# Performance work log

Measured on AMD Instinct MI355X. Metric: run time of the kernel, lower is better.

## Reference

```python
import jax, jax.numpy as jnp
import numpy as np

B, C, H, W = 4, 256, 64, 64

def setup_inputs() -> dict:
    key = jax.random.key(0)
    ks = jax.random.split(key, 6)
    inv = 1.0 / np.sqrt(C)
    return {
        "feature": jax.random.normal(ks[0], (B, C, H, W), dtype=jnp.float32),
        "flow": jax.random.normal(ks[1], (B, 2, H, W), dtype=jnp.float32),
        "q_w": jax.random.uniform(ks[2], (C, C), dtype=jnp.float32, minval=-inv, maxval=inv),
        "q_b": jax.random.uniform(ks[3], (C,), dtype=jnp.float32, minval=-inv, maxval=inv),
        "k_w": jax.random.uniform(ks[4], (C, C), dtype=jnp.float32, minval=-inv, maxval=inv),
        "k_b": jax.random.uniform(ks[5], (C,), dtype=jnp.float32, minval=-inv, maxval=inv),
    }

def reference(feature, flow, q_w, q_b, k_w, k_b):
    b, c, h, w = feature.shape
    # [b,c,h,w] -> [b, h*w, c] tokens
    tok = feature.reshape(b, c, h * w).transpose(0, 2, 1)
    v = flow.reshape(b, 2, h * w).transpose(0, 2, 1)       # [b, hw, 2]
    q = jnp.einsum('bnc,dc->bnd', tok, q_w) + q_b           # Linear(c,c)
    k = jnp.einsum('bnc,dc->bnd', tok, k_w) + k_b
    scale = 1.0 / jnp.sqrt(jnp.asarray(c, dtype=q.dtype))
    scores = jnp.einsum('bld,bsd->bls', q, k) * scale       # [b, hw, hw]
    attn = jax.nn.softmax(scores, axis=-1)                  # dropout_p=0 -> no-op
    out = jnp.einsum('bls,bsv->blv', attn, v)               # [b, hw, 2]
    return out.reshape(b, h, w, 2).transpose(0, 3, 1, 2)    # [b, 2, h, w]
```

## Files before the change

### kernel.cpp

```cpp
#include <hip/hip_runtime.h>
#include <math.h>

#define BB 4
#define CC 256
#define HWN 4096
#define NTOK 16384
#define SCQ 0.09016844136f

typedef __attribute__((ext_vector_type(8))) short short8;
typedef __attribute__((ext_vector_type(4))) float f32x4;
typedef __attribute__((ext_vector_type(2))) float f32x2;
typedef unsigned short ushort_t;

__device__ __forceinline__ ushort_t f2bf(float f) {
    unsigned int u = __float_as_uint(f);
    unsigned int r = (u + 0x7FFFu + ((u >> 16) & 1u)) >> 16;
    return (ushort_t)r;
}
__device__ __forceinline__ unsigned int pack2(float a, float b) {
    return (unsigned int)f2bf(a) | ((unsigned int)f2bf(b) << 16);
}
__device__ __forceinline__ float fexp2(float x) {
#if __has_builtin(__builtin_amdgcn_exp2f)
    return __builtin_amdgcn_exp2f(x);
#else
    return exp2f(x);
#endif
}

__global__ __launch_bounds__(256) void prep_kernel(
    const float* __restrict__ feature,
    const float* __restrict__ q_w, const float* __restrict__ k_w,
    ushort_t* __restrict__ fbuf,
    ushort_t* __restrict__ qwb, ushort_t* __restrict__ kwb,
    float* __restrict__ zbuf)
{
    int bid = blockIdx.x;
    int tid = threadIdx.x;

    if (bid >= 1024) {
        int t = (bid - 1024) * 256 + tid;
        float4 q4 = *(const float4*)&q_w[(size_t)t * 4];
        float4 k4 = *(const float4*)&k_w[(size_t)t * 4];
        unsigned long long qo = (unsigned long long)pack2(q4.x * SCQ, q4.y * SCQ)
                              | ((unsigned long long)pack2(q4.z * SCQ, q4.w * SCQ) << 32);
        unsigned long long ko = (unsigned long long)pack2(k4.x, k4.y)
                              | ((unsigned long long)pack2(k4.z, k4.w) << 32);
        *(unsigned long long*)&qwb[(size_t)t * 4] = qo;
        *(unsigned long long*)&kwb[(size_t)t * 4] = ko;
        zbuf[t] = 0.f; zbuf[t + NTOK] = 0.f; zbuf[t + 2 * NTOK] = 0.f;
        return;
    }

    int b   = bid >> 8;
    int rem = bid & 255;
    int cch = rem >> 6;
    int nch = rem & 63;

    __shared__ float lsA[64][69];

    int cl = tid >> 2, tg = (tid & 3) * 16;
    const float* src = feature + (size_t)(b * CC + cch * 64 + cl) * HWN + nch * 64 + tg;
    *(float4*)&lsA[cl][tg]      = *(const float4*)(src);
    *(float4*)&lsA[cl][tg + 4]  = *(const float4*)(src + 4);
    *(float4*)&lsA[cl][tg + 8]  = *(const float4*)(src + 8);
    *(float4*)&lsA[cl][tg + 12] = *(const float4*)(src + 12);
    __syncthreads();

    int tokw = tid >> 2, c16 = (tid & 3) * 16;
    unsigned int u[8];
    #pragma unroll
    for (int j = 0; j < 8; j++)
        u[j] = pack2(lsA[c16 + 2 * j][tokw], lsA[c16 + 2 * j + 1][tokw]);
    size_t orow = (size_t)(b * HWN + nch * 64 + tokw) * CC + cch * 64 + c16;
    *(uint4*)&fbuf[orow]     = *(uint4*)&u[0];
    *(uint4*)&fbuf[orow + 8] = *(uint4*)&u[4];
}

__global__ __launch_bounds__(256, 2) void proj_kernel(
    const ushort_t* __restrict__ fbuf,
    const ushort_t* __restrict__ qwb, const ushort_t* __restrict__ kwb,
    const float* __restrict__ q_bias, const float* __restrict__ k_bias,
    ushort_t* __restrict__ qb, ushort_t* __restrict__ kb)
{
    int id = blockIdx.x;
    int dh = id >> 8;
    int inner = id & 255;
    int b   = inner & 3;
    int tch = inner >> 2;
    int tok0 = tch * 64;

    int t = threadIdx.x, w = t >> 6, lane = t & 63;
    int n16 = lane & 15, quad = lane >> 4;

    int d0 = dh * 64 + w * 16;

    short8 aq[8], ak[8];
    #pragma unroll
    for (int kc = 0; kc < 8; kc++) {
        size_t off = (size_t)(d0 + n16) * CC + kc * 32 + quad * 8;
        aq[kc] = *(const short8*)&qwb[off];
        ak[kc] = *(const short8*)&kwb[off];
    }
    float bqv[4], bkv[4];
    #pragma unroll
    for (int r = 0; r < 4; r++) {
        bqv[r] = q_bias[d0 + quad * 4 + r] * SCQ;
        bkv[r] = k_bias[d0 + quad * 4 + r];
    }

    #pragma unroll
    for (int tokt = 0; tokt < 4; tokt++) {
        size_t trow = (size_t)(b * HWN + tok0 + tokt * 16 + n16) * CC;
        short8 bf[8];
        #pragma unroll
        for (int kc = 0; kc < 8; kc++)
            bf[kc] = *(const short8*)&fbuf[trow + kc * 32 + quad * 8];
        f32x4 accq = (f32x4){0.f, 0.f, 0.f, 0.f};
        f32x4 acck = (f32x4){0.f, 0.f, 0.f, 0.f};
        #pragma unroll
        for (int kc = 0; kc < 8; kc++) {
            accq = __builtin_amdgcn_mfma_f32_16x16x32_bf16(aq[kc], bf[kc], accq, 0, 0, 0);
            acck = __builtin_amdgcn_mfma_f32_16x16x32_bf16(ak[kc], bf[kc], acck, 0, 0, 0);
        }
        size_t row = trow + d0 + quad * 4;
        ushort4 oq, ok;
        oq.x = f2bf(accq[0] + bqv[0]); oq.y = f2bf(accq[1] + bqv[1]);
        oq.z = f2bf(accq[2] + bqv[2]); oq.w = f2bf(accq[3] + bqv[3]);
        ok.x = f2bf(acck[0] + bkv[0]); ok.y = f2bf(acck[1] + bkv[1]);
        ok.z = f2bf(acck[2] + bkv[2]); ok.w = f2bf(acck[3] + bkv[3]);
        *(ushort4*)&qb[row] = oq;
        *(ushort4*)&kb[row] = ok;
    }
}

__global__ __launch_bounds__(256, 2) void attn_kernel(
    const ushort_t* __restrict__ qb, const ushort_t* __restrict__ kb,
    const float* __restrict__ flow,
    float* __restrict__ den_g, float* __restrict__ nx_g, float* __restrict__ ny_g)
{
    int id = (blockIdx.x & 7) * 128 + (blockIdx.x >> 3);
    int qt = id & 31; id >>= 5;
    int sr = id & 7;  id >>= 3;
    int b = id;

    int t = threadIdx.x;
    int w = t >> 6, lane = t & 63;
    int n16 = lane & 15, quad = lane >> 4;

    int q0 = qt * 128 + w * 32;
    int s_beg = sr * 512;

    const ushort_t* Qb = qb + (size_t)b * HWN * CC;
    const ushort_t* Kb = kb + (size_t)b * HWN * CC;

    __shared__ __align__(16) ushort_t lk[2][8192];
    __shared__ float lflow[1024];

    const float* fx = flow + (size_t)b * 2 * HWN;
    const float* fy = fx + HWN;
    lflow[t]        = fx[s_beg + t];
    lflow[t + 256]  = fx[s_beg + t + 256];
    lflow[t + 512]  = fy[s_beg + t];
    lflow[t + 768]  = fy[s_beg + t + 256];

    short8 qf[2][8];
    #pragma unroll
    for (int tq = 0; tq < 2; tq++)
        #pragma unroll
        for (int c = 0; c < 8; c++)
            qf[tq][c] = *(const short8*)&Qb[(size_t)(q0 + tq * 16 + n16) * CC
                                            + c * 32 + quad * 8];

    int srcoff[4];
    #pragma unroll
    for (int i = 0; i < 4; i++) {
        int G = i * 256 + t;
        int r = G >> 5, j = G & 31;
        srcoff[i] = (r * 32 + (j ^ r)) * 16;
    }
    int p16[8];
    #pragma unroll
    for (int c = 0; c < 8; c++)
        p16[c] = (((c * 4 + quad) ^ n16) & 31) * 16;

    f32x2 den[2][2], nxa[2][2], nya[2][2];
    #pragma unroll
    for (int tq = 0; tq < 2; tq++)
        #pragma unroll
        for (int j = 0; j < 2; j++) {
            den[tq][j] = (f32x2){0.f, 0.f};
            nxa[tq][j] = (f32x2){0.f, 0.f};
            nya[tq][j] = (f32x2){0.f, 0.f};
        }

    {
        const char* gsrc = (const char*)(Kb + (size_t)s_beg * CC);
        char* ldst = (char*)lk[0] + t * 16;
        #pragma unroll
        for (int i = 0; i < 4; i++)
            __builtin_amdgcn_global_load_lds(
                (const __attribute__((address_space(1))) unsigned int*)(gsrc + srcoff[i]),
                (__attribute__((address_space(3))) unsigned int*)(ldst + i * 4096),
                16, 0, 0);
    }

    for (int st = 0; st < 16; st++) {
        __syncthreads();
        if (st + 1 < 16) {
            const char* gsrc = (const char*)(Kb + (size_t)(s_beg + (st + 1) * 32) * CC);
            char* ldst = (char*)lk[(st + 1) & 1] + t * 16;
            #pragma unroll
            for (int i = 0; i < 4; i++)
                __builtin_amdgcn_global_load_lds(
                    (const __attribute__((address_space(1))) unsigned int*)(gsrc + srcoff[i]),
                    (__attribute__((address_space(3))) unsigned int*)(ldst + i * 4096),
                    16, 0, 0);
        }
        const char* base = (const char*)lk[st & 1];

        #pragma unroll
        for (int bt = 0; bt < 2; bt++) {
            int rbase = (bt * 16 + n16) * 512;
            int x16   = bt ? 256 : 0;
            f32x4 a0 = {0.f, 0.f, 0.f, 0.f};
            f32x4 a1 = {0.f, 0.f, 0.f, 0.f};
            #pragma unroll
            for (int c = 0; c < 8; c++) {
                short8 kf = *(const short8*)(base + rbase + (p16[c] ^ x16));
                a0 = __builtin_amdgcn_mfma_f32_16x16x32_bf16(qf[0][c], kf, a0, 0, 0, 0);
                a1 = __builtin_amdgcn_mfma_f32_16x16x32_bf16(qf[1][c], kf, a1, 0, 0, 0);
            }
            int sidx = st * 32 + bt * 16 + n16;
            float vx = lflow[sidx];
            float vy = lflow[512 + sidx];
            f32x2 vx2 = (f32x2){vx, vx};
            f32x2 vy2 = (f32x2){vy, vy};
            #pragma unroll
            for (int tq = 0; tq < 2; tq++) {
                f32x4 a = (tq == 0) ? a0 : a1;
                f32x2 p0 = (f32x2){fexp2(a[0]), fexp2(a[1])};
                f32x2 p1 = (f32x2){fexp2(a[2]), fexp2(a[3])};
                den[tq][0] += p0;
                den[tq][1] += p1;
                nxa[tq][0] = __builtin_elementwise_fma(p0, vx2, nxa[tq][0]);
                nxa[tq][1] = __builtin_elementwise_fma(p1, vx2, nxa[tq][1]);
                nya[tq][0] = __builtin_elementwise_fma(p0, vy2, nya[tq][0]);
                nya[tq][1] = __builtin_elementwise_fma(p1, vy2, nya[tq][1]);
            }
        }
    }

    #pragma unroll
    for (int tq = 0; tq < 2; tq++)
        #pragma unroll
        for (int j = 0; j < 2; j++)
            #pragma unroll
            for (int e = 0; e < 2; e++) {
                float dv = den[tq][j][e];
                float xv = nxa[tq][j][e];
                float yv = nya[tq][j][e];
                #pragma unroll
                for (int off = 8; off >= 1; off >>= 1) {
                    dv += __shfl_down(dv, off, 16);
                    xv += __shfl_down(xv, off, 16);
                    yv += __shfl_down(yv, off, 16);
                }
                if (n16 == 0) {
                    int r = j * 2 + e;
                    int qrow = q0 + tq * 16 + quad * 4 + r;
                    int gi = b * HWN + qrow;
                    atomicAdd(&den_g[gi], dv);
                    atomicAdd(&nx_g[gi],  xv);
                    atomicAdd(&ny_g[gi],  yv);
                }
            }
}

__global__ __launch_bounds__(256) void finalize_kernel(
    const float* __restrict__ den_g, const float* __restrict__ nx_g,
    const float* __restrict__ ny_g, float* __restrict__ out)
{
    int idx = blockIdx.x * 256 + threadIdx.x;
    int b = idx >> 12, n = idx & 4095;
    float inv = 1.0f / den_g[idx];
    out[(size_t)b * 2 * HWN + n]       = nx_g[idx] * inv;
    out[(size_t)b * 2 * HWN + HWN + n] = ny_g[idx] * inv;
}

extern "C" void kernel_launch(void* const* d_in, const int* in_sizes, int n_in,
                              void* d_out, int out_size, void* d_ws, size_t ws_size,
                              hipStream_t stream) {
    const float* feature = (const float*)d_in[0];
    const float* flow    = (const float*)d_in[1];
    const float* q_w     = (const float*)d_in[2];
    const float* q_b     = (const float*)d_in[3];
    const float* k_w     = (const float*)d_in[4];
    const float* k_b     = (const float*)d_in[5];
    float* out = (float*)d_out;

    ushort_t* qbuf = (ushort_t*)d_ws;
    ushort_t* kbuf = qbuf + (size_t)NTOK * CC;
    float* den = (float*)(kbuf + (size_t)NTOK * CC);
    float* nx  = den + NTOK;
    float* ny  = nx + NTOK;
    ushort_t* qwb = (ushort_t*)(ny + NTOK);
    ushort_t* kwb = qwb + (size_t)CC * CC;
    ushort_t* fbuf = kwb + (size_t)CC * CC;

    prep_kernel<<<1088, 256, 0, stream>>>(feature, q_w, k_w, fbuf, qwb, kwb, den);
    proj_kernel<<<1024, 256, 0, stream>>>(fbuf, qwb, kwb, q_b, k_b, qbuf, kbuf);
    attn_kernel<<<1024, 256, 0, stream>>>(qbuf, kbuf, flow, den, nx, ny);
    finalize_kernel<<<64, 256, 0, stream>>>(den, nx, ny, out);
}
```

Baseline: 149.0 us.

## Store Q/K in MFMA-fragment tiled layout and swap operand roles in attention

The projection kernel now writes Q and K bf16 outputs in a pre-tiled fragment layout, so each lane's 16-byte MFMA operand is contiguous. The attention kernel stages a 128-query Q block in LDS once and streams K fragments straight from global into registers, with no double-buffered LDS pipeline. K becomes the A operand, so each lane's accumulator rows map to keys and the per-query reduction becomes a small cross-quad shuffle. The aim is fewer LDS round-trips and barriers and a simpler reduction, at the cost of 64KB of LDS (lower occupancy) and unhidden global-load latency for K.

```diff
diff --git a/kernel.cpp b/kernel.cpp
--- a/kernel.cpp
+++ b/kernel.cpp
@@ -9,7 +9,6 @@
 
 typedef __attribute__((ext_vector_type(8))) short short8;
 typedef __attribute__((ext_vector_type(4))) float f32x4;
-typedef __attribute__((ext_vector_type(2))) float f32x2;
 typedef unsigned short ushort_t;
 
 __device__ __forceinline__ ushort_t f2bf(float f) {
@@ -109,6 +108,10 @@
         bkv[r] = k_bias[d0 + quad * 4 + r];
     }
 
+    int kcq   = d0 >> 5;
+    int quadA = ((d0 >> 4) & 1) * 2 + (quad >> 1);
+    int halfo = quad & 1;
+
     #pragma unroll
     for (int tokt = 0; tokt < 4; tokt++) {
         size_t trow = (size_t)(b * HWN + tok0 + tokt * 16 + n16) * CC;
@@ -123,14 +126,16 @@
             accq = __builtin_amdgcn_mfma_f32_16x16x32_bf16(aq[kc], bf[kc], accq, 0, 0, 0);
             acck = __builtin_amdgcn_mfma_f32_16x16x32_bf16(ak[kc], bf[kc], acck, 0, 0, 0);
         }
-        size_t row = trow + d0 + quad * 4;
         ushort4 oq, ok;
         oq.x = f2bf(accq[0] + bqv[0]); oq.y = f2bf(accq[1] + bqv[1]);
         oq.z = f2bf(accq[2] + bqv[2]); oq.w = f2bf(accq[3] + bqv[3]);
         ok.x = f2bf(acck[0] + bkv[0]); ok.y = f2bf(acck[1] + bkv[1]);
         ok.z = f2bf(acck[2] + bkv[2]); ok.w = f2bf(acck[3] + bkv[3]);
-        *(ushort4*)&qb[row] = oq;
-        *(ushort4*)&kb[row] = ok;
+        int tt_tile = tch * 4 + tokt;
+        size_t gbyte = (((size_t)(b * 256 + tt_tile) * 512) + kcq * 64 + quadA * 16 + n16) * 16
+                       + halfo * 8;
+        *(ushort4*)((char*)qb + gbyte) = oq;
+        *(ushort4*)((char*)kb + gbyte) = ok;
     }
 }
 
@@ -147,14 +152,12 @@
     int t = threadIdx.x;
     int w = t >> 6, lane = t & 63;
     int n16 = lane & 15, quad = lane >> 4;
-
-    int q0 = qt * 128 + w * 32;
+    int qhalf = w & 1, khalf = w >> 1;
+
+    int q0 = qt * 128;
     int s_beg = sr * 512;
 
-    const ushort_t* Qb = qb + (size_t)b * HWN * CC;
-    const ushort_t* Kb = kb + (size_t)b * HWN * CC;
-
-    __shared__ __align__(16) ushort_t lk[2][8192];
+    __shared__ __align__(16) ushort_t qlds[32768];
     __shared__ float lflow[1024];
 
     const float* fx = flow + (size_t)b * 2 * HWN;
@@ -164,117 +167,76 @@
     lflow[t + 512]  = fy[s_beg + t];
     lflow[t + 768]  = fy[s_beg + t + 256];
 
-    short8 qf[2][8];
-    #pragma unroll
-    for (int tq = 0; tq < 2; tq++)
-        #pragma unroll
-        for (int c = 0; c < 8; c++)
-            qf[tq][c] = *(const short8*)&Qb[(size_t)(q0 + tq * 16 + n16) * CC
-                                            + c * 32 + quad * 8];
-
-    int srcoff[4];
-    #pragma unroll
-    for (int i = 0; i < 4; i++) {
-        int G = i * 256 + t;
-        int r = G >> 5, j = G & 31;
-        srcoff[i] = (r * 32 + (j ^ r)) * 16;
-    }
-    int p16[8];
-    #pragma unroll
-    for (int c = 0; c < 8; c++)
-        p16[c] = (((c * 4 + quad) ^ n16) & 31) * 16;
-
-    f32x2 den[2][2], nxa[2][2], nya[2][2];
-    #pragma unroll
-    for (int tq = 0; tq < 2; tq++)
-        #pragma unroll
-        for (int j = 0; j < 2; j++) {
-            den[tq][j] = (f32x2){0.f, 0.f};
-            nxa[tq][j] = (f32x2){0.f, 0.f};
-            nya[tq][j] = (f32x2){0.f, 0.f};
-        }
-
     {
-        const char* gsrc = (const char*)(Kb + (size_t)s_beg * CC);
-        char* ldst = (char*)lk[0] + t * 16;
-        #pragma unroll
-        for (int i = 0; i < 4; i++)
+        const char* qsrc = (const char*)qb + ((size_t)(b * 256 + (q0 >> 4)) * 512) * 16;
+        char* qdst = (char*)qlds;
+        #pragma unroll
+        for (int i = 0; i < 16; i++)
             __builtin_amdgcn_global_load_lds(
-                (const __attribute__((address_space(1))) unsigned int*)(gsrc + srcoff[i]),
-                (__attribute__((address_space(3))) unsigned int*)(ldst + i * 4096),
+                (const __attribute__((address_space(1))) unsigned int*)(qsrc + (i * 256 + t) * 16),
+                (__attribute__((address_space(3))) unsigned int*)(qdst + (i * 256 + t) * 16),
                 16, 0, 0);
     }
-
-    for (int st = 0; st < 16; st++) {
-        __syncthreads();
-        if (st + 1 < 16) {
-            const char* gsrc = (const char*)(Kb + (size_t)(s_beg + (st + 1) * 32) * CC);
-            char* ldst = (char*)lk[(st + 1) & 1] + t * 16;
+    __syncthreads();
+
+    const char* kbase = (const char*)kb
+        + ((size_t)(b * 256 + (s_beg >> 4) + khalf * 16) * 512 + lane) * 16;
+    const char* qldsb = (const char*)qlds + (size_t)qhalf * 4 * 8192 + (size_t)lane * 16;
+
+    float den[4], nxa[4], nya[4];
+    #pragma unroll
+    for (int i = 0; i < 4; i++) { den[i] = 0.f; nxa[i] = 0.f; nya[i] = 0.f; }
+
+    for (int round = 0; round < 8; round++) {
+        short8 kf0[8], kf1[8];
+        #pragma unroll
+        for (int kc = 0; kc < 8; kc++) {
+            kf0[kc] = *(const short8*)(kbase + (round * 2 + 0) * 8192 + kc * 1024);
+            kf1[kc] = *(const short8*)(kbase + (round * 2 + 1) * 8192 + kc * 1024);
+        }
+        int klbase = khalf * 256 + round * 32 + quad * 4;
+        f32x4 vx0 = *(const f32x4*)&lflow[klbase];
+        f32x4 vx1 = *(const f32x4*)&lflow[klbase + 16];
+        f32x4 vy0 = *(const f32x4*)&lflow[512 + klbase];
+        f32x4 vy1 = *(const f32x4*)&lflow[512 + klbase + 16];
+
+        #pragma unroll
+        for (int qtl = 0; qtl < 4; qtl++) {
+            f32x4 a0 = (f32x4){0.f, 0.f, 0.f, 0.f};
+            f32x4 a1 = (f32x4){0.f, 0.f, 0.f, 0.f};
             #pragma unroll
-            for (int i = 0; i < 4; i++)
-                __builtin_amdgcn_global_load_lds(
-                    (const __attribute__((address_space(1))) unsigned int*)(gsrc + srcoff[i]),
-                    (__attribute__((address_space(3))) unsigned int*)(ldst + i * 4096),
-                    16, 0, 0);
-        }
-        const char* base = (const char*)lk[st & 1];
-
-        #pragma unroll
-        for (int bt = 0; bt < 2; bt++) {
-            int rbase = (bt * 16 + n16) * 512;
-            int x16   = bt ? 256 : 0;
-            f32x4 a0 = {0.f, 0.f, 0.f, 0.f};
-            f32x4 a1 = {0.f, 0.f, 0.f, 0.f};
+            for (int kc = 0; kc < 8; kc++) {
+                short8 qf = *(const short8*)(qldsb + qtl * 8192 + kc * 1024);
+                a0 = __builtin_amdgcn_mfma_f32_16x16x32_bf16(kf0[kc], qf, a0, 0, 0, 0);
+                a1 = __builtin_amdgcn_mfma_f32_16x16x32_bf16(kf1[kc], qf, a1, 0, 0, 0);
+            }
+            float d_ = 0.f, x_ = 0.f, y_ = 0.f;
             #pragma unroll
-            for (int c = 0; c < 8; c++) {
-                short8 kf = *(const short8*)(base + rbase + (p16[c] ^ x16));
-                a0 = __builtin_amdgcn_mfma_f32_16x16x32_bf16(qf[0][c], kf, a0, 0, 0, 0);
-                a1 = __builtin_amdgcn_mfma_f32_16x16x32_bf16(qf[1][c], kf, a1, 0, 0, 0);
+            for (int r = 0; r < 4; r++) {
+                float p0 = fexp2(a0[r]);
+                float p1 = fexp2(a1[r]);
+                d_ += p0 + p1;
+                x_ = fmaf(p0, vx0[r], x_); x_ = fmaf(p1, vx1[r], x_);
+                y_ = fmaf(p0, vy0[r], y_); y_ = fmaf(p1, vy1[r], y_);
             }
-            int sidx = st * 32 + bt * 16 + n16;
-            float vx = lflow[sidx];
-            float vy = lflow[512 + sidx];
-            f32x2 vx2 = (f32x2){vx, vx};
-            f32x2 vy2 = (f32x2){vy, vy};
-            #pragma unroll
-            for (int tq = 0; tq < 2; tq++) {
-                f32x4 a = (tq == 0) ? a0 : a1;
-                f32x2 p0 = (f32x2){fexp2(a[0]), fexp2(a[1])};
-                f32x2 p1 = (f32x2){fexp2(a[2]), fexp2(a[3])};
-                den[tq][0] += p0;
-                den[tq][1] += p1;
-                nxa[tq][0] = __builtin_elementwise_fma(p0, vx2, nxa[tq][0]);
-                nxa[tq][1] = __builtin_elementwise_fma(p1, vx2, nxa[tq][1]);
-                nya[tq][0] = __builtin_elementwise_fma(p0, vy2, nya[tq][0]);
-                nya[tq][1] = __builtin_elementwise_fma(p1, vy2, nya[tq][1]);
-            }
-        }
-    }
-
-    #pragma unroll
-    for (int tq = 0; tq < 2; tq++)
-        #pragma unroll
-        for (int j = 0; j < 2; j++)
-            #pragma unroll
-            for (int e = 0; e < 2; e++) {
-                float dv = den[tq][j][e];
-                float xv = nxa[tq][j][e];
-                float yv = nya[tq][j][e];
-                #pragma unroll
-                for (int off = 8; off >= 1; off >>= 1) {
-                    dv += __shfl_down(dv, off, 16);
-                    xv += __shfl_down(xv, off, 16);
-                    yv += __shfl_down(yv, off, 16);
-                }
-                if (n16 == 0) {
-                    int r = j * 2 + e;
-                    int qrow = q0 + tq * 16 + quad * 4 + r;
-                    int gi = b * HWN + qrow;
-                    atomicAdd(&den_g[gi], dv);
-                    atomicAdd(&nx_g[gi],  xv);
-                    atomicAdd(&ny_g[gi],  yv);
-                }
-            }
+            den[qtl] += d_; nxa[qtl] += x_; nya[qtl] += y_;
+        }
+    }
+
+    #pragma unroll
+    for (int qtl = 0; qtl < 4; qtl++) {
+        float dv = den[qtl], xv = nxa[qtl], yv = nya[qtl];
+        dv += __shfl_down(dv, 32); dv += __shfl_down(dv, 16);
+        xv += __shfl_down(xv, 32); xv += __shfl_down(xv, 16);
+        yv += __shfl_down(yv, 32); yv += __shfl_down(yv, 16);
+        if (lane < 16) {
+            int qrow = q0 + qhalf * 64 + qtl * 16 + n16;
+            int gi = b * HWN + qrow;
+            atomicAdd(&den_g[gi], dv);
+            atomicAdd(&nx_g[gi],  xv);
+            atomicAdd(&ny_g[gi],  yv);
+        }
+    }
 }
 
 __global__ __launch_bounds__(256) void finalize_kernel(
```

Measured after the change: 146.1 us. -2.0%, faster.
